# Performance work log

Hardware: AMD Instinct MI355X
Metric: run time of the kernel (lower is better)

## Reference

```python
import jax, jax.numpy as jnp
import numpy as np

B, N, D, H, C = 16, 512, 256, 8, 16
DK = D // H  # per-head dim


def gelu(x):
    return jax.nn.gelu(x, approximate=False)  # torch F.gelu default (erf)


def mha(x, Wq, Wk, Wv, Wo):
    # x: [N, D] treated as a length-N token sequence; standard scaled-dot MHA
    n = x.shape[0]
    q = (x @ Wq).reshape(n, H, DK)
    k = (x @ Wk).reshape(n, H, DK)
    v = (x @ Wv).reshape(n, H, DK)
    scores = jnp.einsum('nhd,mhd->hnm', q, k) / jnp.sqrt(jnp.asarray(DK, x.dtype))
    attn = jax.nn.softmax(scores, axis=-1)
    out = jnp.einsum('hnm,mhd->nhd', attn, v).reshape(n, H * DK)
    return out @ Wo


def setup_inputs() -> dict:
    key = jax.random.key(0)
    ks = jax.random.split(key, 16)
    scale = 1.0 / np.sqrt(D)
    w = lambda i, shape: jax.random.normal(ks[i], shape, jnp.float32) * scale
    return {
        'embeddings': jax.random.normal(ks[0], (B, N, D), jnp.float32),
        'labels': jax.random.randint(ks[1], (B, N), 0, C),
        'Wq0': w(2, (D, D)), 'Wk0': w(3, (D, D)), 'Wv0': w(4, (D, D)), 'Wo0': w(5, (D, D)),
        'Wq1': w(6, (D, D)), 'Wk1': w(7, (D, D)), 'Wv1': w(8, (D, D)), 'Wo1': w(9, (D, D)),
        'res_W': w(10, (D, D)), 'res_b': jnp.zeros((D,), jnp.float32),
        'ff_W1': w(11, (2 * D, D)), 'ff_b1': jnp.zeros((D,), jnp.float32),
        'ff_W2': w(12, (D, D)), 'ff_b2': jnp.zeros((D,), jnp.float32),
    }


def reference(embeddings, labels, Wq0, Wk0, Wv0, Wo0, Wq1, Wk1, Wv1, Wo1,
              res_W, res_b, ff_W1, ff_b1, ff_W2, ff_b2):
    # one-hot class membership; torch.unique over randint labels == arange(C)
    onehot = (labels[..., None] == jnp.arange(C)).astype(jnp.float32)  # [B,N,C]

    def episode(e, m):
        # e: [N, D]  m: [N, C]
        x = mha(e, Wq0, Wk0, Wv0, Wo0)
        x = gelu(x)
        x = mha(x, Wq1, Wk1, Wv1, Wo1)
        aggr = gelu(jnp.mean(x, axis=0))          # [D]  set-level summary
        aggr = aggr @ res_W + res_b               # res_linear
        e2 = jnp.concatenate([jnp.broadcast_to(aggr, (N, D)), e], axis=1)  # [N,2D]
        e2 = gelu(e2)
        e2 = gelu(e2 @ ff_W1 + ff_b1) @ ff_W2 + ff_b2  # ff_linear -> [N,D]
        # pairwise sample similarities with self-exclusion
        S = e2 @ e2.T                              # [N,N]
        S = S * (1.0 - jnp.eye(N, dtype=S.dtype))
        counts = jnp.sum(m, axis=0)                # [C]
        norm = counts[None, :] - m                 # leave-one-out class size [N,C]
        return (S.T @ m) / norm                    # per-class masked mean -> [N,C]

    return jax.vmap(episode)(embeddings, onehot)
```

## Files before the change

kernel.cpp:

```cpp
#include <hip/hip_runtime.h>

#define BB 16
#define NN 512
#define DD 256
#define HH 8
#define CC 16

typedef unsigned short u16;
using short8 = __attribute__((ext_vector_type(8))) short;
using f32x4  = __attribute__((ext_vector_type(4))) float;

__device__ __forceinline__ float gelu_f(float x) {
    return 0.5f * x * (1.0f + erff(x * 0.70710678118654752f));
}
__device__ __forceinline__ u16 f2bf(float f) {
    unsigned int u = __float_as_uint(f);
    unsigned int r = u + 0x7FFFu + ((u >> 16) & 1u);
    return (u16)(r >> 16);
}
__device__ __forceinline__ void gld16(const u16* g, const u16* l) {
    __builtin_amdgcn_global_load_lds(
        (const __attribute__((address_space(1))) unsigned int*)g,
        (__attribute__((address_space(3))) unsigned int*)l, 16, 0, 0);
}

#define QSCALE 0.25505412f

__device__ __forceinline__ float mv256(const float* __restrict__ a,
                                       const float* __restrict__ W, int d)
{
    float acc[8] = {0.f, 0.f, 0.f, 0.f, 0.f, 0.f, 0.f, 0.f};
    for (int k = 0; k < 256; k += 8) {
#pragma unroll
        for (int j = 0; j < 8; ++j)
            acc[j] += a[k + j] * W[(size_t)(k + j) * 256 + d];
    }
    return ((acc[0] + acc[1]) + (acc[2] + acc[3])) + ((acc[4] + acc[5]) + (acc[6] + acc[7]));
}

template<int ACT, int HAS_B, int HAS_T, int OUT_F32, int CS>
__global__ __launch_bounds__(256) void gemm64(
    const u16* __restrict__ A, const u16* __restrict__ W,
    u16* __restrict__ O, float* __restrict__ OF,
    const float* __restrict__ bias, const float* __restrict__ tvec,
    const int* __restrict__ labels, float* __restrict__ gsum)
{
    __shared__ __align__(16) u16 As[64 * 32];
    __shared__ __align__(16) u16 Bs[64 * 32];
    const int tid = threadIdx.x, wave = tid >> 6, lane = tid & 63;
    const int col = lane & 15, quad = lane >> 4;
    const int mbase = blockIdx.x * 64;
    const int nbase = blockIdx.y * 64;
    const int srow = lane >> 2, skk = (lane & 3) * 8;
    const int mh = (wave & 1) * 32, nh = (wave >> 1) * 32;

    f32x4 acc[2][2];
#pragma unroll
    for (int i = 0; i < 2; ++i)
#pragma unroll
        for (int j = 0; j < 2; ++j) acc[i][j] = (f32x4){0.f, 0.f, 0.f, 0.f};

    for (int k0 = 0; k0 < DD; k0 += 32) {
        gld16(A + (size_t)(mbase + wave * 16 + srow) * DD + k0 + skk, &As[wave * 512]);
        gld16(W + (size_t)(nbase + wave * 16 + srow) * DD + k0 + skk, &Bs[wave * 512]);
        __syncthreads();
        short8 af[2], bfr[2];
#pragma unroll
        for (int i = 0; i < 2; ++i) af[i]  = *(const short8*)&As[(mh + i * 16 + col) * 32 + quad * 8];
#pragma unroll
        for (int j = 0; j < 2; ++j) bfr[j] = *(const short8*)&Bs[(nh + j * 16 + col) * 32 + quad * 8];
#pragma unroll
        for (int i = 0; i < 2; ++i)
#pragma unroll
            for (int j = 0; j < 2; ++j)
                acc[i][j] = __builtin_amdgcn_mfma_f32_16x16x32_bf16(af[i], bfr[j], acc[i][j], 0, 0, 0);
        __syncthreads();
    }

    const int b = mbase >> 9;
    if constexpr (!CS) {
#pragma unroll
        for (int i = 0; i < 2; ++i) {
#pragma unroll
            for (int j = 0; j < 2; ++j) {
                const int ccol = nbase + nh + j * 16 + col;
#pragma unroll
                for (int r = 0; r < 4; ++r) {
                    const int crow = mbase + mh + i * 16 + quad * 4 + r;
                    float v = acc[i][j][r];
                    if (HAS_B) v += bias[ccol];
                    if (HAS_T) v += tvec[b * DD + ccol];
                    if (ACT)   v = gelu_f(v);
                    if (OUT_F32) OF[(size_t)crow * DD + ccol] = v;
                    else         O[(size_t)crow * DD + ccol] = f2bf(v);
                }
            }
        }
    } else {
        __shared__ float Fs[64][65];
        __shared__ float gs[4][CC][64];
        __shared__ int lab2[64];
        if (tid < 64) lab2[tid] = labels[mbase + tid];
#pragma unroll
        for (int i = 0; i < 2; ++i) {
#pragma unroll
            for (int j = 0; j < 2; ++j) {
                const int lcol = nh + j * 16 + col;
                const int ccol = nbase + lcol;
#pragma unroll
                for (int r = 0; r < 4; ++r) {
                    const int lrow = mh + i * 16 + quad * 4 + r;
                    float v = acc[i][j][r];
                    if (HAS_B) v += bias[ccol];
                    if (HAS_T) v += tvec[b * DD + ccol];
                    if (ACT)   v = gelu_f(v);
                    OF[(size_t)(mbase + lrow) * DD + ccol] = v;
                    Fs[lrow][lcol] = v;
                }
            }
        }
        __syncthreads();
        float a[CC];
#pragma unroll
        for (int c = 0; c < CC; ++c) a[c] = 0.f;
#pragma unroll
        for (int n = 0; n < 16; ++n) {
            const float v = Fs[wave * 16 + n][lane];
            const int lb = lab2[wave * 16 + n];
#pragma unroll
            for (int c = 0; c < CC; ++c) a[c] += (lb == c) ? v : 0.f;
        }
#pragma unroll
        for (int c = 0; c < CC; ++c) gs[wave][c][lane] = a[c];
        __syncthreads();
#pragma unroll
        for (int i = 0; i < 4; ++i) {
            const int c = wave * 4 + i;
            atomicAdd(&gsum[((size_t)b * CC + c) * DD + nbase + lane],
                      gs[0][c][lane] + gs[1][c][lane] + gs[2][c][lane] + gs[3][c][lane]);
        }
    }
}

__global__ __launch_bounds__(256) void gemm_qkv(
    const u16* __restrict__ A,
    const u16* __restrict__ W0, const u16* __restrict__ W1, const u16* __restrict__ W2,
    u16* __restrict__ O0, u16* __restrict__ O1, u16* __restrict__ O2)
{
    __shared__ __align__(16) u16 As[64 * 32];
    __shared__ __align__(16) u16 Bs[64 * 32];
    const int tid = threadIdx.x, wave = tid >> 6, lane = tid & 63;
    const int col = lane & 15, quad = lane >> 4;
    const int mbase = blockIdx.x * 64;
    const int sel = blockIdx.y >> 2;
    const int nbase = (blockIdx.y & 3) * 64;
    const u16* W = (sel == 0) ? W0 : ((sel == 1) ? W1 : W2);
    u16* O = (sel == 0) ? O0 : ((sel == 1) ? O1 : O2);
    const int srow = lane >> 2, skk = (lane & 3) * 8;
    const int mh = (wave & 1) * 32, nh = (wave >> 1) * 32;

    f32x4 acc[2][2];
#pragma unroll
    for (int i = 0; i < 2; ++i)
#pragma unroll
        for (int j = 0; j < 2; ++j) acc[i][j] = (f32x4){0.f, 0.f, 0.f, 0.f};

    for (int k0 = 0; k0 < DD; k0 += 32) {
        gld16(A + (size_t)(mbase + wave * 16 + srow) * DD + k0 + skk, &As[wave * 512]);
        gld16(W + (size_t)(nbase + wave * 16 + srow) * DD + k0 + skk, &Bs[wave * 512]);
        __syncthreads();
        short8 af[2], bfr[2];
#pragma unroll
        for (int i = 0; i < 2; ++i) af[i]  = *(const short8*)&As[(mh + i * 16 + col) * 32 + quad * 8];
#pragma unroll
        for (int j = 0; j < 2; ++j) bfr[j] = *(const short8*)&Bs[(nh + j * 16 + col) * 32 + quad * 8];
#pragma unroll
        for (int i = 0; i < 2; ++i)
#pragma unroll
            for (int j = 0; j < 2; ++j)
                acc[i][j] = __builtin_amdgcn_mfma_f32_16x16x32_bf16(af[i], bfr[j], acc[i][j], 0, 0, 0);
        __syncthreads();
    }

    const int b = mbase >> 9;
#pragma unroll
    for (int i = 0; i < 2; ++i) {
#pragma unroll
        for (int j = 0; j < 2; ++j) {
            const int ccol = nbase + nh + j * 16 + col;
            const int tok0 = (mbase & 511) + mh + i * 16 + quad * 4;
            const int head = ccol >> 5, dk = ccol & 31;
            if (sel == 2) {
                ushort4 pk;
                pk.x = f2bf(acc[i][j][0]); pk.y = f2bf(acc[i][j][1]);
                pk.z = f2bf(acc[i][j][2]); pk.w = f2bf(acc[i][j][3]);
                *(ushort4*)&O[(((size_t)b * HH + head) * 32 + dk) * NN + tok0] = pk;
            } else {
#pragma unroll
                for (int r = 0; r < 4; ++r) {
                    float v = acc[i][j][r];
                    if (sel == 0) v *= QSCALE;
                    O[(((size_t)b * HH + head) * NN + tok0 + r) * 32 + dk] = f2bf(v);
                }
            }
        }
    }
}

template<int COLSUM>
__global__ __launch_bounds__(256) void attn_mfma(
    const u16* __restrict__ Qh, const u16* __restrict__ Kh,
    const u16* __restrict__ VT, u16* __restrict__ O,
    float* __restrict__ partial)
{
    __shared__ __align__(16) u16 Vt[32 * 520];
    __shared__ __align__(16) u16 Pc[4][16 * 32];
    __shared__ float cs[4][32];
    const int tid = threadIdx.x, wave = tid >> 6, lane = tid & 63;
    const int col = lane & 15, quad = lane >> 4;
    const int gid = blockIdx.x;
    const int qb = gid >> 7, bh = gid & 127;
    const int q0 = qb * 64 + wave * 16;

    const u16* vsrc = VT + (size_t)bh * 32 * NN;
#pragma unroll
    for (int i = 0; i < 8; ++i) {
        const int row = wave + i * 4;
        gld16(vsrc + (size_t)row * NN + lane * 8, &Vt[row * 520]);
    }
    const short8 aq = *(const short8*)(Qh + ((size_t)bh * NN + q0 + col) * 32 + quad * 8);
    __syncthreads();

    const u16* ksrc = Kh + (size_t)bh * NN * 32;
    float l[4] = {0.f, 0.f, 0.f, 0.f};
    f32x4 oacc[2];
    oacc[0] = (f32x4){0.f, 0.f, 0.f, 0.f};
    oacc[1] = (f32x4){0.f, 0.f, 0.f, 0.f};

    short8 bkp[2];
#pragma unroll
    for (int k2 = 0; k2 < 2; ++k2)
        bkp[k2] = *(const short8*)(ksrc + (size_t)(k2 * 16 + col) * 32 + quad * 8);

    for (int g = 0; g < 16; ++g) {
        short8 bk0 = bkp[0], bk1 = bkp[1];
        if (g < 15) {
#pragma unroll
            for (int k2 = 0; k2 < 2; ++k2)
                bkp[k2] = *(const short8*)(ksrc + (size_t)((g * 2 + 2 + k2) * 16 + col) * 32 + quad * 8);
        }
#pragma unroll
        for (int k2 = 0; k2 < 2; ++k2) {
            f32x4 z = {0.f, 0.f, 0.f, 0.f};
            const f32x4 s = __builtin_amdgcn_mfma_f32_16x16x32_bf16(aq, k2 ? bk1 : bk0, z, 0, 0, 0);
#pragma unroll
            for (int r = 0; r < 4; ++r) {
                const float p = exp2f(s[r]);
                l[r] += p;
                Pc[wave][(quad * 4 + r) * 32 + (((k2 * 2 + (col >> 3)) ^ quad) << 3) + (col & 7)] = f2bf(p);
            }
        }
        const short8 ap = *(const short8*)&Pc[wave][col * 32 + ((quad ^ (col >> 2)) << 3)];
#pragma unroll
        for (int nt = 0; nt < 2; ++nt) {
            const short8 bv = *(const short8*)&Vt[(nt * 16 + col) * 520 + g * 32 + quad * 8];
            oacc[nt] = __builtin_amdgcn_mfma_f32_16x16x32_bf16(ap, bv, oacc[nt], 0, 0, 0);
        }
    }
#pragma unroll
    for (int r = 0; r < 4; ++r) {
        l[r] += __shfl_xor(l[r], 1, 64);
        l[r] += __shfl_xor(l[r], 2, 64);
        l[r] += __shfl_xor(l[r], 4, 64);
        l[r] += __shfl_xor(l[r], 8, 64);
    }
    if (COLSUM) {
        float sv[2] = {0.f, 0.f};
#pragma unroll
        for (int nt = 0; nt < 2; ++nt) {
#pragma unroll
            for (int r = 0; r < 4; ++r) sv[nt] += oacc[nt][r] / l[r];
            sv[nt] += __shfl_xor(sv[nt], 16, 64);
            sv[nt] += __shfl_xor(sv[nt], 32, 64);
        }
        if (lane < 16) { cs[wave][col] = sv[0]; cs[wave][16 + col] = sv[1]; }
        __syncthreads();
        if (tid < 32)
            partial[(size_t)(bh * 8 + qb) * 32 + tid] =
                cs[0][tid] + cs[1][tid] + cs[2][tid] + cs[3][tid];
    } else {
        const int b = bh >> 3, h = bh & 7;
        u16* obase = O + ((size_t)b * NN) * DD + h * 32;
#pragma unroll
        for (int nt = 0; nt < 2; ++nt)
#pragma unroll
            for (int r = 0; r < 4; ++r)
                obase[(size_t)(q0 + quad * 4 + r) * DD + nt * 16 + col] = f2bf(oacc[nt][r] / l[r]);
    }
}

__global__ __launch_bounds__(256) void convert_all(
    const float* __restrict__ e, u16* __restrict__ E, u16* __restrict__ G,
    const float* s0, const float* s1, const float* s2, const float* s3,
    const float* s4, const float* s5, const float* s6, const float* s7,
    const float* s8, u16* __restrict__ Wt, float* __restrict__ gsum)
{
    const int bx = blockIdx.x;
    if (bx < 2048) {
        const size_t i = ((size_t)bx * 256 + threadIdx.x) * 4;
        const float4 v = *(const float4*)(e + i);
        ushort4 ev, gv;
        ev.x = f2bf(v.x); ev.y = f2bf(v.y); ev.z = f2bf(v.z); ev.w = f2bf(v.w);
        gv.x = f2bf(gelu_f(v.x)); gv.y = f2bf(gelu_f(v.y));
        gv.z = f2bf(gelu_f(v.z)); gv.w = f2bf(gelu_f(v.w));
        *(ushort4*)(E + i) = ev;
        *(ushort4*)(G + i) = gv;
    } else if (bx < 2192) {
        const int w = bx - 2048;
        const int my = w >> 4, kb = (w & 15) * 16;
        const int n = threadIdx.x;
        const float* S;
        switch (my) {
            case 0: S = s0; break; case 1: S = s1; break; case 2: S = s2; break;
            case 3: S = s3; break; case 4: S = s4; break; case 5: S = s5; break;
            case 6: S = s6; break; case 7: S = s7; break; default: S = s8; break;
        }
        u16* Dst = Wt + (size_t)my * 65536;
        for (int r = 0; r < 16; ++r) {
            const int k = kb + r;
            Dst[(size_t)n * 256 + k] = f2bf(S[(size_t)k * 256 + n]);
        }
    } else {
        const int z = bx - 2192;
        const float4 zz = {0.f, 0.f, 0.f, 0.f};
        *(float4*)(gsum + (size_t)z * 1024 + threadIdx.x * 4) = zz;
    }
}

__global__ __launch_bounds__(256) void aggr_v2(
    const float* __restrict__ partial, const float* __restrict__ Wo1f,
    const float* __restrict__ resW, const float* __restrict__ resb,
    const float* __restrict__ W1, const int* __restrict__ labels,
    float* __restrict__ tvec, float* __restrict__ counts)
{
    const int b = blockIdx.x, d = threadIdx.x;
    __shared__ float a0[256], a1[256], a2[256];
    __shared__ int hist[CC];
    if (d < CC) hist[d] = 0;
    const int h = d >> 5, d32 = d & 31;
    float s = 0.f;
#pragma unroll
    for (int qb = 0; qb < 8; ++qb)
        s += partial[(size_t)(((b * 8 + h) * 8) + qb) * 32 + d32];
    a0[d] = s * (1.0f / NN);
    __syncthreads();
    atomicAdd(&hist[labels[b * NN + d]], 1);
    atomicAdd(&hist[labels[b * NN + 256 + d]], 1);
    a1[d] = gelu_f(mv256(a0, Wo1f, d));
    __syncthreads();
    a2[d] = gelu_f(mv256(a1, resW, d) + resb[d]);
    __syncthreads();
    tvec[b * 256 + d] = mv256(a2, W1, d);
    if (d < CC) counts[b * CC + d] = (float)hist[d];
}

__global__ __launch_bounds__(256) void out_kernel(
    const float* __restrict__ F, const int* __restrict__ labels,
    const float* __restrict__ g, const float* __restrict__ counts,
    float* __restrict__ out)
{
    const int b = blockIdx.y;
    const int wave = threadIdx.x >> 6, lane = threadIdx.x & 63;
    const int n = blockIdx.x * 4 + wave;
    const float* fn = F + ((size_t)b * NN + n) * DD;
    const float* gb = g + (size_t)b * CC * DD;
    float fv[4];
#pragma unroll
    for (int i = 0; i < 4; ++i) fv[i] = fn[lane * 4 + i];
    float selfdot = 0.f;
#pragma unroll
    for (int i = 0; i < 4; ++i) selfdot += fv[i] * fv[i];
    float accs[CC];
#pragma unroll
    for (int c = 0; c < CC; ++c) {
        float sacc = 0.f;
#pragma unroll
        for (int i = 0; i < 4; ++i) sacc += fv[i] * gb[c * DD + lane * 4 + i];
        accs[c] = sacc;
    }
    for (int off = 32; off; off >>= 1) {
        selfdot += __shfl_xor(selfdot, off, 64);
#pragma unroll
        for (int c = 0; c < CC; ++c) accs[c] += __shfl_xor(accs[c], off, 64);
    }
    if (lane < CC) {
        const int c = lane;
        const int same = (labels[b * NN + n] == c) ? 1 : 0;
        const float num = accs[c] - (same ? selfdot : 0.f);
        const float den = counts[b * CC + c] - (float)same;
        out[((size_t)b * NN + n) * CC + c] = num / den;
    }
}

extern "C" void kernel_launch(void* const* d_in, const int* in_sizes, int n_in,
                              void* d_out, int out_size, void* d_ws, size_t ws_size,
                              hipStream_t stream)
{
    const float* emb    = (const float*)d_in[0];
    const int*   labels = (const int*)  d_in[1];
    const float* Wo1f = (const float*)d_in[9];
    const float* resW = (const float*)d_in[10];
    const float* resb = (const float*)d_in[11];
    const float* ffW1 = (const float*)d_in[12];
    const float* ffb1 = (const float*)d_in[13];
    const float* ffb2 = (const float*)d_in[15];
    float* out = (float*)d_out;

    const size_t SBE = (size_t)BB * NN * DD;
    u16* BUF0 = (u16*)d_ws;
    u16* BUF1 = BUF0 + SBE;
    u16* BUF2 = BUF1 + SBE;
    u16* BUF3 = BUF2 + SBE;
    u16* BUF4 = BUF3 + SBE;
    u16* BUF5 = BUF4 + SBE;
    u16* Wt   = BUF5 + SBE;
    float* F      = (float*)(Wt + 9 * 65536);
    float* tvec   = F + SBE;
    float* partial= tvec + BB * 256;
    float* gsum   = partial + 128 * 8 * 32;
    float* counts = gsum + (size_t)BB * CC * DD;

    convert_all<<<2048 + 144 + 64, 256, 0, stream>>>(
        emb, BUF0, BUF1,
        (const float*)d_in[2], (const float*)d_in[3], (const float*)d_in[4],
        (const float*)d_in[5], (const float*)d_in[6], (const float*)d_in[7],
        (const float*)d_in[8], ffW1 + 256 * 256, (const float*)d_in[14], Wt,
        gsum);
    gemm_qkv<<<dim3(128, 12), 256, 0, stream>>>(
        BUF0, Wt, Wt + 65536, Wt + 2 * 65536, BUF2, BUF3, BUF4);
    attn_mfma<0><<<1024, 256, 0, stream>>>(BUF2, BUF3, BUF4, BUF5, nullptr);
    gemm64<1,0,0,0,0><<<dim3(128, 4), 256, 0, stream>>>(
        BUF5, Wt + 3 * 65536, BUF0, nullptr, nullptr, nullptr, nullptr, nullptr);
    gemm_qkv<<<dim3(128, 12), 256, 0, stream>>>(
        BUF0, Wt + 4 * 65536, Wt + 5 * 65536, Wt + 6 * 65536, BUF2, BUF3, BUF4);
    attn_mfma<1><<<1024, 256, 0, stream>>>(BUF2, BUF3, BUF4, nullptr, partial);
    aggr_v2<<<BB, 256, 0, stream>>>(partial, Wo1f, resW, resb, ffW1, labels, tvec, counts);
    gemm64<1,1,1,0,0><<<dim3(128, 4), 256, 0, stream>>>(
        BUF1, Wt + 7 * 65536, BUF3, nullptr, ffb1, tvec, nullptr, nullptr);
    gemm64<0,1,0,1,1><<<dim3(128, 4), 256, 0, stream>>>(
        BUF3, Wt + 8 * 65536, nullptr, F, ffb2, nullptr, labels, gsum);
    out_kernel<<<dim3(128, BB), 256, 0, stream>>>(F, labels, gsum, counts, out);
}
```

Measured before the change: 199.6 us.

## Software-pipeline attention P tile, split aggr matvecs across 1024 threads, rework output kernel

Three separate changes. The attention inner loop now computes the next group's softmax probabilities into registers one step ahead, so the exp and score MFMAs overlap with the PV MFMAs. The aggregation kernel grows to 1024 threads, each computing a 64-wide K slice of each 256x256 matvec, followed by a shared-memory reduction, which cuts the serial chain in that 16-block kernel. The output kernel is restructured so each thread computes one (row, class) dot product with float4 loads instead of wave-wide shuffle reductions. The cost is more barriers and redundant F row reads.

```diff
diff --git a/kernel.cpp b/kernel.cpp
--- a/kernel.cpp
+++ b/kernel.cpp
@@ -25,18 +25,6 @@
 }
 
 #define QSCALE 0.25505412f
-
-__device__ __forceinline__ float mv256(const float* __restrict__ a,
-                                       const float* __restrict__ W, int d)
-{
-    float acc[8] = {0.f, 0.f, 0.f, 0.f, 0.f, 0.f, 0.f, 0.f};
-    for (int k = 0; k < 256; k += 8) {
-#pragma unroll
-        for (int j = 0; j < 8; ++j)
-            acc[j] += a[k + j] * W[(size_t)(k + j) * 256 + d];
-    }
-    return ((acc[0] + acc[1]) + (acc[2] + acc[3])) + ((acc[4] + acc[5]) + (acc[6] + acc[7]));
-}
 
 template<int ACT, int HAS_B, int HAS_T, int OUT_F32, int CS>
 __global__ __launch_bounds__(256) void gemm64(
@@ -241,26 +229,44 @@
 #pragma unroll
     for (int k2 = 0; k2 < 2; ++k2)
         bkp[k2] = *(const short8*)(ksrc + (size_t)(k2 * 16 + col) * 32 + quad * 8);
+    u16 pr[8];
+    {
+        const f32x4 z = {0.f, 0.f, 0.f, 0.f};
+        const f32x4 s0 = __builtin_amdgcn_mfma_f32_16x16x32_bf16(aq, bkp[0], z, 0, 0, 0);
+        const f32x4 s1 = __builtin_amdgcn_mfma_f32_16x16x32_bf16(aq, bkp[1], z, 0, 0, 0);
+#pragma unroll
+        for (int r = 0; r < 4; ++r) {
+            const float p0 = exp2f(s0[r]); l[r] += p0; pr[r]     = f2bf(p0);
+            const float p1 = exp2f(s1[r]); l[r] += p1; pr[4 + r] = f2bf(p1);
+        }
+    }
+#pragma unroll
+    for (int k2 = 0; k2 < 2; ++k2)
+        bkp[k2] = *(const short8*)(ksrc + (size_t)((2 + k2) * 16 + col) * 32 + quad * 8);
 
     for (int g = 0; g < 16; ++g) {
-        short8 bk0 = bkp[0], bk1 = bkp[1];
+#pragma unroll
+        for (int k2 = 0; k2 < 2; ++k2)
+#pragma unroll
+            for (int r = 0; r < 4; ++r)
+                Pc[wave][(quad * 4 + r) * 32 + (((k2 * 2 + (col >> 3)) ^ quad) << 3) + (col & 7)] = pr[k2 * 4 + r];
+        const short8 ap = *(const short8*)&Pc[wave][col * 32 + ((quad ^ (col >> 2)) << 3)];
         if (g < 15) {
-#pragma unroll
-            for (int k2 = 0; k2 < 2; ++k2)
-                bkp[k2] = *(const short8*)(ksrc + (size_t)((g * 2 + 2 + k2) * 16 + col) * 32 + quad * 8);
-        }
-#pragma unroll
-        for (int k2 = 0; k2 < 2; ++k2) {
-            f32x4 z = {0.f, 0.f, 0.f, 0.f};
-            const f32x4 s = __builtin_amdgcn_mfma_f32_16x16x32_bf16(aq, k2 ? bk1 : bk0, z, 0, 0, 0);
+            const short8 bk0 = bkp[0], bk1 = bkp[1];
+            if (g < 14) {
+#pragma unroll
+                for (int k2 = 0; k2 < 2; ++k2)
+                    bkp[k2] = *(const short8*)(ksrc + (size_t)((2 * (g + 2) + k2) * 16 + col) * 32 + quad * 8);
+            }
+            const f32x4 z = {0.f, 0.f, 0.f, 0.f};
+            const f32x4 s0 = __builtin_amdgcn_mfma_f32_16x16x32_bf16(aq, bk0, z, 0, 0, 0);
+            const f32x4 s1 = __builtin_amdgcn_mfma_f32_16x16x32_bf16(aq, bk1, z, 0, 0, 0);
 #pragma unroll
             for (int r = 0; r < 4; ++r) {
-                const float p = exp2f(s[r]);
-                l[r] += p;
-                Pc[wave][(quad * 4 + r) * 32 + (((k2 * 2 + (col >> 3)) ^ quad) << 3) + (col & 7)] = f2bf(p);
+                const float p0 = exp2f(s0[r]); l[r] += p0; pr[r]     = f2bf(p0);
+                const float p1 = exp2f(s1[r]); l[r] += p1; pr[4 + r] = f2bf(p1);
             }
         }
-        const short8 ap = *(const short8*)&Pc[wave][col * 32 + ((quad ^ (col >> 2)) << 3)];
 #pragma unroll
         for (int nt = 0; nt < 2; ++nt) {
             const short8 bv = *(const short8*)&Vt[(nt * 16 + col) * 520 + g * 32 + quad * 8];
@@ -337,69 +343,82 @@
     }
 }
 
-__global__ __launch_bounds__(256) void aggr_v2(
+__device__ __forceinline__ float mvslice(const float* __restrict__ a,
+                                         const float* __restrict__ W,
+                                         int d, int k0)
+{
+    float acc[4] = {0.f, 0.f, 0.f, 0.f};
+    for (int k = k0; k < k0 + 64; k += 4) {
+#pragma unroll
+        for (int j = 0; j < 4; ++j)
+            acc[j] += a[k + j] * W[(size_t)(k + j) * 256 + d];
+    }
+    return (acc[0] + acc[1]) + (acc[2] + acc[3]);
+}
+
+__global__ __launch_bounds__(1024) void aggr_v3(
     const float* __restrict__ partial, const float* __restrict__ Wo1f,
     const float* __restrict__ resW, const float* __restrict__ resb,
     const float* __restrict__ W1, const int* __restrict__ labels,
     float* __restrict__ tvec, float* __restrict__ counts)
 {
-    const int b = blockIdx.x, d = threadIdx.x;
-    __shared__ float a0[256], a1[256], a2[256];
+    const int b = blockIdx.x, t = threadIdx.x;
+    const int d = t & 255, sl = t >> 8;
+    __shared__ float av[256];
+    __shared__ float red[4][256];
     __shared__ int hist[CC];
-    if (d < CC) hist[d] = 0;
+    if (t < CC) hist[t] = 0;
     const int h = d >> 5, d32 = d & 31;
     float s = 0.f;
 #pragma unroll
-    for (int qb = 0; qb < 8; ++qb)
-        s += partial[(size_t)(((b * 8 + h) * 8) + qb) * 32 + d32];
-    a0[d] = s * (1.0f / NN);
-    __syncthreads();
-    atomicAdd(&hist[labels[b * NN + d]], 1);
-    atomicAdd(&hist[labels[b * NN + 256 + d]], 1);
-    a1[d] = gelu_f(mv256(a0, Wo1f, d));
-    __syncthreads();
-    a2[d] = gelu_f(mv256(a1, resW, d) + resb[d]);
-    __syncthreads();
-    tvec[b * 256 + d] = mv256(a2, W1, d);
-    if (d < CC) counts[b * CC + d] = (float)hist[d];
-}
-
-__global__ __launch_bounds__(256) void out_kernel(
+    for (int q = 0; q < 2; ++q)
+        s += partial[(size_t)(((b * 8 + h) * 8) + sl * 2 + q) * 32 + d32];
+    red[sl][d] = s;
+    __syncthreads();
+    if (t < 512) atomicAdd(&hist[labels[b * NN + t]], 1);
+    if (sl == 0) av[d] = (red[0][d] + red[1][d] + red[2][d] + red[3][d]) * (1.0f / NN);
+    __syncthreads();
+    red[sl][d] = mvslice(av, Wo1f, d, sl * 64);
+    __syncthreads();
+    if (sl == 0) av[d] = gelu_f(red[0][d] + red[1][d] + red[2][d] + red[3][d]);
+    __syncthreads();
+    red[sl][d] = mvslice(av, resW, d, sl * 64);
+    __syncthreads();
+    if (sl == 0) av[d] = gelu_f(red[0][d] + red[1][d] + red[2][d] + red[3][d] + resb[d]);
+    __syncthreads();
+    red[sl][d] = mvslice(av, W1, d, sl * 64);
+    __syncthreads();
+    if (sl == 0) {
+        tvec[b * 256 + d] = red[0][d] + red[1][d] + red[2][d] + red[3][d];
+        if (d < CC) counts[b * CC + d] = (float)hist[d];
+    }
+}
+
+__global__ __launch_bounds__(256) void out_v2(
     const float* __restrict__ F, const int* __restrict__ labels,
     const float* __restrict__ g, const float* __restrict__ counts,
     float* __restrict__ out)
 {
     const int b = blockIdx.y;
-    const int wave = threadIdx.x >> 6, lane = threadIdx.x & 63;
-    const int n = blockIdx.x * 4 + wave;
+    const int n = blockIdx.x * 16 + (threadIdx.x >> 4);
+    const int c = threadIdx.x & 15;
     const float* fn = F + ((size_t)b * NN + n) * DD;
-    const float* gb = g + (size_t)b * CC * DD;
-    float fv[4];
-#pragma unroll
-    for (int i = 0; i < 4; ++i) fv[i] = fn[lane * 4 + i];
-    float selfdot = 0.f;
-#pragma unroll
-    for (int i = 0; i < 4; ++i) selfdot += fv[i] * fv[i];
-    float accs[CC];
-#pragma unroll
-    for (int c = 0; c < CC; ++c) {
-        float sacc = 0.f;
-#pragma unroll
-        for (int i = 0; i < 4; ++i) sacc += fv[i] * gb[c * DD + lane * 4 + i];
-        accs[c] = sacc;
-    }
-    for (int off = 32; off; off >>= 1) {
-        selfdot += __shfl_xor(selfdot, off, 64);
-#pragma unroll
-        for (int c = 0; c < CC; ++c) accs[c] += __shfl_xor(accs[c], off, 64);
-    }
-    if (lane < CC) {
-        const int c = lane;
-        const int same = (labels[b * NN + n] == c) ? 1 : 0;
-        const float num = accs[c] - (same ? selfdot : 0.f);
-        const float den = counts[b * CC + c] - (float)same;
-        out[((size_t)b * NN + n) * CC + c] = num / den;
-    }
+    const float* gc = g + ((size_t)b * CC + c) * DD;
+    float d0 = 0.f, d1 = 0.f, s0 = 0.f, s1 = 0.f;
+    for (int k = 0; k < DD; k += 8) {
+        const float4 f0 = *(const float4*)(fn + k);
+        const float4 f1 = *(const float4*)(fn + k + 4);
+        const float4 g0 = *(const float4*)(gc + k);
+        const float4 g1 = *(const float4*)(gc + k + 4);
+        d0 += f0.x * g0.x + f0.y * g0.y + f0.z * g0.z + f0.w * g0.w;
+        d1 += f1.x * g1.x + f1.y * g1.y + f1.z * g1.z + f1.w * g1.w;
+        s0 += f0.x * f0.x + f0.y * f0.y + f0.z * f0.z + f0.w * f0.w;
+        s1 += f1.x * f1.x + f1.y * f1.y + f1.z * f1.z + f1.w * f1.w;
+    }
+    const int same = (labels[b * NN + n] == c) ? 1 : 0;
+    const float num = (d0 + d1) - (same ? (s0 + s1) : 0.f);
+    const float den = counts[b * CC + c] - (float)same;
+    out[((size_t)b * NN + n) * CC + c] = num / den;
 }
 
 extern "C" void kernel_launch(void* const* d_in, const int* in_sizes, int n_in,
@@ -444,10 +463,10 @@
     gemm_qkv<<<dim3(128, 12), 256, 0, stream>>>(
         BUF0, Wt + 4 * 65536, Wt + 5 * 65536, Wt + 6 * 65536, BUF2, BUF3, BUF4);
     attn_mfma<1><<<1024, 256, 0, stream>>>(BUF2, BUF3, BUF4, nullptr, partial);
-    aggr_v2<<<BB, 256, 0, stream>>>(partial, Wo1f, resW, resb, ffW1, labels, tvec, counts);
+    aggr_v3<<<BB, 1024, 0, stream>>>(partial, Wo1f, resW, resb, ffW1, labels, tvec, counts);
     gemm64<1,1,1,0,0><<<dim3(128, 4), 256, 0, stream>>>(
         BUF1, Wt + 7 * 65536, BUF3, nullptr, ffb1, tvec, nullptr, nullptr);
     gemm64<0,1,0,1,1><<<dim3(128, 4), 256, 0, stream>>>(
         BUF3, Wt + 8 * 65536, nullptr, F, ffb2, nullptr, labels, gsum);
-    out_kernel<<<dim3(128, BB), 256, 0, stream>>>(F, labels, gsum, counts, out);
-}
+    out_v2<<<dim3(32, BB), 256, 0, stream>>>(F, labels, gsum, counts, out);
+}
```

After: 217.1 us. 1.09x slower.
